# Performance work log

Hardware: AMD Instinct MI355X
Metric: run time of the kernel (lower is better)

The kernel has to match this reference:

```python
import jax, jax.numpy as jnp
import numpy as np

SPARSITY_PROB = 0.1
CAUSAL = True
B, H, S, D = 2, 16, 2048, 64


def _make_mask(key, seq_len, sparsity_prob, causal):
    # random_mask = rand < p, optionally AND causal tril, then force diagonal True
    m = jax.random.uniform(key, (seq_len, seq_len)) < sparsity_prob
    if causal:
        m = m & jnp.tril(jnp.ones((seq_len, seq_len), dtype=bool))
    idx = jnp.arange(seq_len)
    m = m.at[idx, idx].set(True)
    return m


def setup_inputs() -> dict:
    key = jax.random.key(0)
    kq, kk, kv, km = jax.random.split(key, 4)
    query = jax.random.normal(kq, (B, H, S, D), dtype=jnp.float32)
    k_ = jax.random.normal(kk, (B, H, S, D), dtype=jnp.float32)
    v_ = jax.random.normal(kv, (B, H, S, D), dtype=jnp.float32)
    mask = _make_mask(km, S, SPARSITY_PROB, CAUSAL)
    return {"query": query, "key": k_, "value": v_, "mask": mask}


def reference(query, key, value, mask):
    # Masked attention: softmax over the selected positions of each row is
    # mathematically identical to the per-row gather+softmax in the original.
    # mask: [S, S] bool, shared across batch and heads; every row has at least
    # the diagonal True, so no fully-masked rows.
    head_dim = query.shape[-1]
    scale = 1.0 / jnp.sqrt(jnp.asarray(head_dim, dtype=query.dtype))
    scores = jnp.einsum("bhqd,bhkd->bhqk", query, key) * scale  # [B,H,S,S]
    scores = jnp.where(mask[None, None, :, :], scores, -jnp.inf)
    attn = jax.nn.softmax(scores, axis=-1)
    return jnp.einsum("bhqk,bhkd->bhqd", attn, value)
```

## Files before the change

kernel.cpp:

```cpp
#include <hip/hip_runtime.h>
#include <hip/hip_bf16.h>

#define SEQ 2048
#define HD 64
#define NBH 32
#define SCALE 0.125f
#define QSC 0.18033688011112042f

typedef __attribute__((ext_vector_type(4)))  float    f32x4;
typedef __attribute__((ext_vector_type(16))) float    f32x16;
typedef __attribute__((ext_vector_type(8)))  short    bf16x8;
typedef __attribute__((ext_vector_type(4)))  unsigned u32x4;

__device__ inline short f2bf(float f) {
    unsigned u = __builtin_bit_cast(unsigned, f);
    unsigned r = u + 0x7FFFu + ((u >> 16) & 1u);
    return (short)(r >> 16);
}

__device__ inline unsigned cvt2(float lo, float hi) {
    unsigned d;
    asm("v_cvt_pk_bf16_f32 %0, %1, %2" : "=v"(d) : "v"(lo), "v"(hi));
    return d;
}

__global__ void detect_mask_kernel(const unsigned char* __restrict__ m, int n, int* flag) {
    if (threadIdx.x == 0) *flag = (m[n - 1] != 0) ? 1 : 4;
}

__global__ __launch_bounds__(256)
void prep_kernel(const unsigned char* __restrict__ m, const int* __restrict__ flag,
                 const float* __restrict__ K, const float* __restrict__ V,
                 unsigned* __restrict__ bits, short* __restrict__ Kb,
                 short* __restrict__ Vt) {
    __shared__ short t[64][65];
    const int b = blockIdx.x, tid = threadIdx.x;
    if (b < 512) {
        const int idx = b * 256 + tid;
        const int row = idx >> 6, w = idx & 63;
        const size_t base = (size_t)row * SEQ + w * 32;
        unsigned word = 0;
        if (*flag == 1) {
            #pragma unroll
            for (int i = 0; i < 32; ++i) word |= (unsigned)(m[base + i] != 0) << i;
        } else {
            const unsigned* m32 = (const unsigned*)m;
            #pragma unroll
            for (int i = 0; i < 32; ++i) word |= (unsigned)(m32[base + i] != 0) << i;
        }
        bits[(size_t)w * SEQ + row] = word;
    } else if (b < 2560) {
        const int g = (b - 512) * 256 + tid;
        const size_t i = (size_t)g * 8;
        f32x4 a = *(const f32x4*)(K + i);
        f32x4 c = *(const f32x4*)(K + i + 4);
        bf16x8 o;
        #pragma unroll
        for (int j = 0; j < 4; ++j) { o[j] = f2bf(a[j]); o[4 + j] = f2bf(c[j]); }
        const int row = g >> 3;
        const int c8  = g & 7;
        const int bh  = row >> 11;
        const int r   = row & 2047;
        const int tt  = r >> 5;
        const int la  = r & 31;
        *(bf16x8*)(Kb + ((size_t)bh * 64 + tt) * 2048 + (c8 * 32 + la) * 8) = o;
    } else {
        const int bb = b - 2560;
        const int s0 = (bb & 31) * 64, bh = bb >> 5;
        const float* Vb = V + (size_t)bh * SEQ * HD;
        const int sr = tid >> 6, d = tid & 63;
        #pragma unroll
        for (int i = 0; i < 16; ++i) {
            const int s = i * 4 + sr;
            t[s][d] = f2bf(Vb[(size_t)(s0 + s) * HD + d]);
        }
        __syncthreads();
        short* o = Vt + (size_t)bh * HD * SEQ;
        const int dr = tid >> 6, sl = tid & 63;
        #pragma unroll
        for (int i = 0; i < 16; ++i) {
            const int dd = i * 4 + dr;
            const int s = s0 + sl;
            const int k = s & 31;
            const int p = (k & ~12) | ((k & 8) >> 1) | ((k & 4) << 1);
            const int mm = ((dd >> 5) << 1) | (p >> 4);
            const int hh = (p >> 3) & 1;
            o[(size_t)(s >> 5) * 2048 + ((mm * 2 + hh) * 32 + (dd & 31)) * 8 + (p & 7)] = t[sl][dd];
        }
    }
}

__global__ __launch_bounds__(256, 2)
void attn_shared_kernel(const float* __restrict__ Q, const short* __restrict__ Kb,
                        const short* __restrict__ Vt, const unsigned* __restrict__ bitsT,
                        float* __restrict__ Out) {
    __shared__ __align__(16) short kbuf[2][2][2048];
    __shared__ __align__(16) short vbuf[2][2][2048];
    __shared__ short oacc[4][32][72];

    const int id   = blockIdx.x;
    const int bh   = id & 31;
    const int qg   = (id < 256) ? (15 - (id >> 5)) : ((id - 256) >> 5);
    const int tid  = threadIdx.x;
    const int wid  = tid >> 6;
    const int lane = tid & 63;
    const int la   = lane & 31;
    const int h    = lane >> 5;
    const int q0w  = qg * 128 + wid * 32;
    const int nt   = qg * 4 + 4;
    const size_t base = (size_t)bh * SEQ * HD;

    bf16x8 qf[4];
    {
        const float* qp = Q + base + (size_t)(q0w + la) * HD + h * 8;
        #pragma unroll
        for (int j = 0; j < 4; ++j) {
            f32x4 a0 = *(const f32x4*)(qp + j * 16);
            f32x4 a1 = *(const f32x4*)(qp + j * 16 + 4);
            #pragma unroll
            for (int i = 0; i < 4; ++i) {
                qf[j][i]     = f2bf(a0[i] * QSC);
                qf[j][4 + i] = f2bf(a1[i] * QSC);
            }
        }
    }

    f32x16 acc_o0 = {0,0,0,0,0,0,0,0,0,0,0,0,0,0,0,0};
    f32x16 acc_o1 = {0,0,0,0,0,0,0,0,0,0,0,0,0,0,0,0};
    float l_run = 0.f;

    const short* Ktg = Kb + (size_t)bh * 64 * 2048;
    const short* Vtg = Vt + (size_t)bh * 64 * 2048;
    const unsigned* bq = bitsT + q0w + la;
    const int bp = 4 * h;

    auto body = [&](const short* kb, const short* vb, unsigned mwx) {
        bf16x8 kfa = *(const bf16x8*)(kb + lane * 8);
        bf16x8 kfb = *(const bf16x8*)(kb + 512 + lane * 8);
        bf16x8 kfc = *(const bf16x8*)(kb + 1024 + lane * 8);
        bf16x8 kfd = *(const bf16x8*)(kb + 1536 + lane * 8);
        bf16x8 vf00 = *(const bf16x8*)(vb + lane * 8);
        bf16x8 vf01 = *(const bf16x8*)(vb + 512 + lane * 8);
        bf16x8 vf10 = *(const bf16x8*)(vb + 1024 + lane * 8);
        bf16x8 vf11 = *(const bf16x8*)(vb + 1536 + lane * 8);

        f32x16 sA = {0,0,0,0,0,0,0,0,0,0,0,0,0,0,0,0};
        f32x16 sB = {0,0,0,0,0,0,0,0,0,0,0,0,0,0,0,0};
        __builtin_amdgcn_s_setprio(1);
        sA = __builtin_amdgcn_mfma_f32_32x32x16_bf16(kfa, qf[0], sA, 0, 0, 0);
        sB = __builtin_amdgcn_mfma_f32_32x32x16_bf16(kfc, qf[2], sB, 0, 0, 0);
        sA = __builtin_amdgcn_mfma_f32_32x32x16_bf16(kfb, qf[1], sA, 0, 0, 0);
        sB = __builtin_amdgcn_mfma_f32_32x32x16_bf16(kfd, qf[3], sB, 0, 0, 0);
        __builtin_amdgcn_s_setprio(0);
        f32x16 s = sA + sB;

        #pragma unroll
        for (int r = 0; r < 16; ++r) {
            float e = __builtin_amdgcn_exp2f(s[r]);
            s[r] = ((mwx >> (bp + (r & 3) + 8 * (r >> 2))) & 1u) ? e : 0.f;
        }
        float ps = ((s[0] + s[1]) + (s[2] + s[3])) + ((s[4] + s[5]) + (s[6] + s[7]));
        ps += ((s[8] + s[9]) + (s[10] + s[11])) + ((s[12] + s[13]) + (s[14] + s[15]));
        l_run += ps;

        u32x4 t1 = {cvt2(s[0], s[1]),  cvt2(s[2], s[3]),
                    cvt2(s[4], s[5]),  cvt2(s[6], s[7])};
        u32x4 t2 = {cvt2(s[8], s[9]),  cvt2(s[10], s[11]),
                    cvt2(s[12], s[13]), cvt2(s[14], s[15])};
        bf16x8 pb1 = __builtin_bit_cast(bf16x8, t1);
        bf16x8 pb2 = __builtin_bit_cast(bf16x8, t2);

        __builtin_amdgcn_s_setprio(1);
        acc_o0 = __builtin_amdgcn_mfma_f32_32x32x16_bf16(vf00, pb1, acc_o0, 0, 0, 0);
        acc_o1 = __builtin_amdgcn_mfma_f32_32x32x16_bf16(vf10, pb1, acc_o1, 0, 0, 0);
        acc_o0 = __builtin_amdgcn_mfma_f32_32x32x16_bf16(vf01, pb2, acc_o0, 0, 0, 0);
        acc_o1 = __builtin_amdgcn_mfma_f32_32x32x16_bf16(vf11, pb2, acc_o1, 0, 0, 0);
        __builtin_amdgcn_s_setprio(0);
    };

    {
        bf16x8 k0 = *(const bf16x8*)(Ktg + (size_t)tid * 8);
        bf16x8 k1 = *(const bf16x8*)(Ktg + 2048 + (size_t)tid * 8);
        bf16x8 v0 = *(const bf16x8*)(Vtg + (size_t)tid * 8);
        bf16x8 v1 = *(const bf16x8*)(Vtg + 2048 + (size_t)tid * 8);
        *(bf16x8*)(&kbuf[0][0][0] + tid * 8) = k0;
        *(bf16x8*)(&kbuf[0][1][0] + tid * 8) = k1;
        *(bf16x8*)(&vbuf[0][0][0] + tid * 8) = v0;
        *(bf16x8*)(&vbuf[0][1][0] + tid * 8) = v1;
    }
    unsigned mw0 = bq[0];
    unsigned mw1 = bq[SEQ];

    int cur = 0;
    for (int t = 0; t < nt; t += 2) {
        __syncthreads();

        const int tn0 = (t + 2 < nt) ? t + 2 : t;
        const int tn1 = (t + 3 < nt) ? t + 3 : t;
        bf16x8 sk0 = *(const bf16x8*)(Ktg + (size_t)tn0 * 2048 + tid * 8);
        bf16x8 sk1 = *(const bf16x8*)(Ktg + (size_t)tn1 * 2048 + tid * 8);
        bf16x8 sv0 = *(const bf16x8*)(Vtg + (size_t)tn0 * 2048 + tid * 8);
        bf16x8 sv1 = *(const bf16x8*)(Vtg + (size_t)tn1 * 2048 + tid * 8);
        unsigned nmw0 = bq[(size_t)tn0 * SEQ];
        unsigned nmw1 = bq[(size_t)tn1 * SEQ];

        body(&kbuf[cur][0][0], &vbuf[cur][0][0], mw0);
        body(&kbuf[cur][1][0], &vbuf[cur][1][0], mw1);

        *(bf16x8*)(&kbuf[cur ^ 1][0][0] + tid * 8) = sk0;
        *(bf16x8*)(&kbuf[cur ^ 1][1][0] + tid * 8) = sk1;
        *(bf16x8*)(&vbuf[cur ^ 1][0][0] + tid * 8) = sv0;
        *(bf16x8*)(&vbuf[cur ^ 1][1][0] + tid * 8) = sv1;

        mw0 = nmw0; mw1 = nmw1;
        cur ^= 1;
    }

    {
        const float l_full = l_run + __shfl_xor(l_run, 32);
        const float invw = 1.f / l_full;
        unsigned short* orow = (unsigned short*)&oacc[wid][la][0];
        #pragma unroll
        for (int g = 0; g < 4; ++g) {
            const int d0 = 8 * g + 4 * h;
            unsigned w0 = cvt2(acc_o0[4 * g + 0] * invw, acc_o0[4 * g + 1] * invw);
            unsigned w1 = cvt2(acc_o0[4 * g + 2] * invw, acc_o0[4 * g + 3] * invw);
            unsigned w2 = cvt2(acc_o1[4 * g + 0] * invw, acc_o1[4 * g + 1] * invw);
            unsigned w3 = cvt2(acc_o1[4 * g + 2] * invw, acc_o1[4 * g + 3] * invw);
            *(unsigned*)&orow[d0]      = w0;
            *(unsigned*)&orow[d0 + 2]  = w1;
            *(unsigned*)&orow[d0 + 32] = w2;
            *(unsigned*)&orow[d0 + 34] = w3;
        }
    }
    __syncthreads();

    {
        const int q  = tid >> 3;
        const int dc = (tid & 7) * 8;
        #pragma unroll
        for (int k = 0; k < 4; ++k) {
            u32x4 pk = *(const u32x4*)&oacc[k][q][dc];
            float o[8];
            #pragma unroll
            for (int j = 0; j < 4; ++j) {
                o[2 * j]     = __builtin_bit_cast(float, (pk[j] & 0xFFFFu) << 16);
                o[2 * j + 1] = __builtin_bit_cast(float, pk[j] & 0xFFFF0000u);
            }
            float* op = Out + base + (size_t)(qg * 128 + k * 32 + q) * HD + dc;
            f32x4 o0v = {o[0], o[1], o[2], o[3]};
            f32x4 o1v = {o[4], o[5], o[6], o[7]};
            *(f32x4*)op       = o0v;
            *(f32x4*)(op + 4) = o1v;
        }
    }
}

__global__ __launch_bounds__(256)
void attn_kernel(const float* __restrict__ Q, const float* __restrict__ K,
                 const float* __restrict__ V, const unsigned char* __restrict__ mask,
                 const int* __restrict__ flag, float* __restrict__ Out) {
    __shared__ short plds[4][16][40];
    const int esz  = *flag;
    const int bh   = blockIdx.y;
    const int wid  = threadIdx.x >> 6;
    const int lane = threadIdx.x & 63;
    const int l16  = lane & 15;
    const int hi   = lane >> 4;
    const int q0   = blockIdx.x * 64 + wid * 16;
    const size_t base = (size_t)bh * SEQ * HD;
    const float* Qb = Q + base;
    const float* Kb = K + base;
    const float* Vb = V + base;
    const unsigned int* mask32 = (const unsigned int*)mask;
    bf16x8 qf[2];
    {
        const float* qp = Qb + (size_t)(q0 + l16) * HD + hi * 8;
        f32x4 a0 = *(const f32x4*)(qp);
        f32x4 a1 = *(const f32x4*)(qp + 4);
        f32x4 a2 = *(const f32x4*)(qp + 32);
        f32x4 a3 = *(const f32x4*)(qp + 36);
        #pragma unroll
        for (int i = 0; i < 4; ++i) {
            qf[0][i] = f2bf(a0[i]); qf[0][4 + i] = f2bf(a1[i]);
            qf[1][i] = f2bf(a2[i]); qf[1][4 + i] = f2bf(a3[i]);
        }
    }
    f32x4 acc_o[4] = {f32x4{0,0,0,0}, f32x4{0,0,0,0}, f32x4{0,0,0,0}, f32x4{0,0,0,0}};
    float m_run[4], l_run[4];
    #pragma unroll
    for (int j = 0; j < 4; ++j) { m_run[j] = -__builtin_inff(); l_run[j] = 0.f; }
    const int kv_end = q0 + 16;
    for (int kv = 0; kv < kv_end; kv += 32) {
        f32x4 acc_s[2] = {f32x4{0,0,0,0}, f32x4{0,0,0,0}};
        #pragma unroll
        for (int t = 0; t < 2; ++t) {
            const float* kp = Kb + (size_t)(kv + 16 * t + l16) * HD + hi * 8;
            f32x4 b0 = *(const f32x4*)(kp);
            f32x4 b1 = *(const f32x4*)(kp + 4);
            f32x4 b2 = *(const f32x4*)(kp + 32);
            f32x4 b3 = *(const f32x4*)(kp + 36);
            bf16x8 kf0, kf1;
            #pragma unroll
            for (int i = 0; i < 4; ++i) {
                kf0[i] = f2bf(b0[i]); kf0[4 + i] = f2bf(b1[i]);
                kf1[i] = f2bf(b2[i]); kf1[4 + i] = f2bf(b3[i]);
            }
            acc_s[t] = __builtin_amdgcn_mfma_f32_16x16x32_bf16(qf[0], kf0, acc_s[t], 0, 0, 0);
            acc_s[t] = __builtin_amdgcn_mfma_f32_16x16x32_bf16(qf[1], kf1, acc_s[t], 0, 0, 0);
        }
        float s[2][4];
        #pragma unroll
        for (int t = 0; t < 2; ++t) {
            const int k = kv + 16 * t + l16;
            #pragma unroll
            for (int j = 0; j < 4; ++j) {
                const int qrow = q0 + hi * 4 + j;
                const size_t midx = (size_t)qrow * SEQ + k;
                const bool mv = (esz == 1) ? (mask[midx] != 0) : (mask32[midx] != 0);
                s[t][j] = mv ? acc_s[t][j] * SCALE : -__builtin_inff();
            }
        }
        float mnew[4], r[4];
        #pragma unroll
        for (int j = 0; j < 4; ++j) {
            float v = fmaxf(s[0][j], s[1][j]);
            #pragma unroll
            for (int off = 1; off < 16; off <<= 1) v = fmaxf(v, __shfl_xor(v, off));
            mnew[j] = fmaxf(m_run[j], v);
            r[j] = (m_run[j] > -__builtin_inff()) ? __expf(m_run[j] - mnew[j]) : 0.f;
        }
        float p[2][4];
        #pragma unroll
        for (int j = 0; j < 4; ++j) {
            float ps = 0.f;
            #pragma unroll
            for (int t = 0; t < 2; ++t) {
                p[t][j] = (s[t][j] > -__builtin_inff()) ? __expf(s[t][j] - mnew[j]) : 0.f;
                ps += p[t][j];
            }
            #pragma unroll
            for (int off = 1; off < 16; off <<= 1) ps += __shfl_xor(ps, off);
            l_run[j] = l_run[j] * r[j] + ps;
            m_run[j] = mnew[j];
            #pragma unroll
            for (int t2 = 0; t2 < 4; ++t2) acc_o[t2][j] *= r[j];
        }
        #pragma unroll
        for (int t = 0; t < 2; ++t)
            #pragma unroll
            for (int j = 0; j < 4; ++j)
                plds[wid][hi * 4 + j][16 * t + l16] = f2bf(p[t][j]);
        bf16x8 pa = *(bf16x8*)&plds[wid][l16][hi * 8];
        #pragma unroll
        for (int t2 = 0; t2 < 4; ++t2) {
            const float* vp = Vb + (size_t)(kv + hi * 8) * HD + 16 * t2 + l16;
            bf16x8 vf;
            #pragma unroll
            for (int i = 0; i < 8; ++i) vf[i] = f2bf(vp[(size_t)i * HD]);
            acc_o[t2] = __builtin_amdgcn_mfma_f32_16x16x32_bf16(pa, vf, acc_o[t2], 0, 0, 0);
        }
    }
    #pragma unroll
    for (int j = 0; j < 4; ++j) {
        const float inv = 1.f / l_run[j];
        const int qrow = q0 + hi * 4 + j;
        float* op = Out + base + (size_t)qrow * HD + l16;
        #pragma unroll
        for (int t2 = 0; t2 < 4; ++t2) op[16 * t2] = acc_o[t2][j] * inv;
    }
}

extern "C" void kernel_launch(void* const* d_in, const int* in_sizes, int n_in,
                              void* d_out, int out_size, void* d_ws, size_t ws_size,
                              hipStream_t stream) {
    const float* Q = (const float*)d_in[0];
    const float* K = (const float*)d_in[1];
    const float* V = (const float*)d_in[2];
    const unsigned char* mask = (const unsigned char*)d_in[3];

    const size_t bitsB = (size_t)SEQ * (SEQ / 32) * 4;
    const size_t kvB   = (size_t)NBH * SEQ * HD * 2;
    const size_t need  = bitsB + 2 * kvB + 256;

    if (ws_size >= need) {
        unsigned* bits = (unsigned*)d_ws;
        short* Kb = (short*)((char*)d_ws + bitsB);
        short* Vt = (short*)((char*)d_ws + bitsB + kvB);
        int* flag = (int*)((char*)d_ws + bitsB + 2 * kvB);

        detect_mask_kernel<<<dim3(1), dim3(64), 0, stream>>>(mask, in_sizes[3], flag);
        prep_kernel<<<dim3(3584), dim3(256), 0, stream>>>(mask, flag, K, V, bits, Kb, Vt);
        attn_shared_kernel<<<dim3(512), dim3(256), 0, stream>>>(Q, Kb, Vt, bits, (float*)d_out);
    } else {
        int* flag = (int*)d_ws;
        detect_mask_kernel<<<dim3(1), dim3(64), 0, stream>>>(mask, in_sizes[3], flag);
        attn_kernel<<<dim3(SEQ / 64, NBH), dim3(256), 0, stream>>>(Q, K, V, mask, flag, (float*)d_out);
    }
}
```

Before: 58.43 us.

## Split attention KV range into halves with separate reduction kernel

Adds a split-KV attention path: each query group's causal key range is divided into two halves processed by separate blocks (1024 blocks, occupancy hint 4). Each block writes partial normalized outputs in bf16 and row sums to workspace, and a reduce kernel combines them weighted by the sums. The aim is more parallelism and better load balance across CUs for the causal workload. In exchange it adds an extra kernel launch, workspace traffic, and bf16 rounding of the partial outputs. The softmax skips the running max and relies on the prescaled exp2 scores staying bounded.

```diff
diff --git a/kernel.cpp b/kernel.cpp
--- a/kernel.cpp
+++ b/kernel.cpp
@@ -90,6 +90,213 @@
     }
 }
 
+__global__ __launch_bounds__(256, 4)
+void attn_half_kernel(const float* __restrict__ Q, const short* __restrict__ Kb,
+                      const short* __restrict__ Vt, const unsigned* __restrict__ bitsT,
+                      short* __restrict__ Oh_ws, float* __restrict__ l_ws) {
+    __shared__ __align__(16) short pool[16384];
+    short* kpool = pool;
+    short* vpool = pool + 8192;
+
+    const int id   = blockIdx.x;
+    const int bh   = id & 31;
+    const int s8   = (id >> 5) & 7;
+    const int g    = id >> 8;
+    int qg, half;
+    if (g == 0)      { qg = 15 - s8; half = 0; }
+    else if (g == 1) { qg = 8 + s8;  half = 1; }
+    else if (g == 2) { qg = 7 - s8;  half = 0; }
+    else             { qg = s8;      half = 1; }
+
+    const int tid  = threadIdx.x;
+    const int wid  = tid >> 6;
+    const int lane = tid & 63;
+    const int la   = lane & 31;
+    const int h    = lane >> 5;
+    const int q0w  = qg * 128 + wid * 32;
+    const int htiles = 2 * qg + 2;
+    const int tstart = half * htiles;
+    const int tend   = tstart + htiles;
+    const size_t base = (size_t)bh * SEQ * HD;
+
+    bf16x8 qf[4];
+    {
+        const float* qp = Q + base + (size_t)(q0w + la) * HD + h * 8;
+        #pragma unroll
+        for (int j = 0; j < 4; ++j) {
+            f32x4 a0 = *(const f32x4*)(qp + j * 16);
+            f32x4 a1 = *(const f32x4*)(qp + j * 16 + 4);
+            #pragma unroll
+            for (int i = 0; i < 4; ++i) {
+                qf[j][i]     = f2bf(a0[i] * QSC);
+                qf[j][4 + i] = f2bf(a1[i] * QSC);
+            }
+        }
+    }
+
+    f32x16 acc_o0 = {0,0,0,0,0,0,0,0,0,0,0,0,0,0,0,0};
+    f32x16 acc_o1 = {0,0,0,0,0,0,0,0,0,0,0,0,0,0,0,0};
+    float l_run = 0.f;
+
+    const short* Ktg = Kb + (size_t)bh * 64 * 2048;
+    const short* Vtg = Vt + (size_t)bh * 64 * 2048;
+    const unsigned* bq = bitsT + q0w + la;
+    const int bp = 4 * h;
+
+    auto body = [&](const short* kb, const short* vb, unsigned mwx) {
+        bf16x8 kfa = *(const bf16x8*)(kb + lane * 8);
+        bf16x8 kfb = *(const bf16x8*)(kb + 512 + lane * 8);
+        bf16x8 kfc = *(const bf16x8*)(kb + 1024 + lane * 8);
+        bf16x8 kfd = *(const bf16x8*)(kb + 1536 + lane * 8);
+        bf16x8 vf00 = *(const bf16x8*)(vb + lane * 8);
+        bf16x8 vf01 = *(const bf16x8*)(vb + 512 + lane * 8);
+        bf16x8 vf10 = *(const bf16x8*)(vb + 1024 + lane * 8);
+        bf16x8 vf11 = *(const bf16x8*)(vb + 1536 + lane * 8);
+
+        f32x16 sA = {0,0,0,0,0,0,0,0,0,0,0,0,0,0,0,0};
+        f32x16 sB = {0,0,0,0,0,0,0,0,0,0,0,0,0,0,0,0};
+        __builtin_amdgcn_s_setprio(1);
+        sA = __builtin_amdgcn_mfma_f32_32x32x16_bf16(kfa, qf[0], sA, 0, 0, 0);
+        sB = __builtin_amdgcn_mfma_f32_32x32x16_bf16(kfc, qf[2], sB, 0, 0, 0);
+        sA = __builtin_amdgcn_mfma_f32_32x32x16_bf16(kfb, qf[1], sA, 0, 0, 0);
+        sB = __builtin_amdgcn_mfma_f32_32x32x16_bf16(kfd, qf[3], sB, 0, 0, 0);
+        __builtin_amdgcn_s_setprio(0);
+        f32x16 s = sA + sB;
+
+        #pragma unroll
+        for (int r = 0; r < 16; ++r) {
+            float e = __builtin_amdgcn_exp2f(s[r]);
+            s[r] = ((mwx >> (bp + (r & 3) + 8 * (r >> 2))) & 1u) ? e : 0.f;
+        }
+        float ps = ((s[0] + s[1]) + (s[2] + s[3])) + ((s[4] + s[5]) + (s[6] + s[7]));
+        ps += ((s[8] + s[9]) + (s[10] + s[11])) + ((s[12] + s[13]) + (s[14] + s[15]));
+        l_run += ps;
+
+        u32x4 t1 = {cvt2(s[0], s[1]),  cvt2(s[2], s[3]),
+                    cvt2(s[4], s[5]),  cvt2(s[6], s[7])};
+        u32x4 t2 = {cvt2(s[8], s[9]),  cvt2(s[10], s[11]),
+                    cvt2(s[12], s[13]), cvt2(s[14], s[15])};
+        bf16x8 pb1 = __builtin_bit_cast(bf16x8, t1);
+        bf16x8 pb2 = __builtin_bit_cast(bf16x8, t2);
+
+        __builtin_amdgcn_s_setprio(1);
+        acc_o0 = __builtin_amdgcn_mfma_f32_32x32x16_bf16(vf00, pb1, acc_o0, 0, 0, 0);
+        acc_o1 = __builtin_amdgcn_mfma_f32_32x32x16_bf16(vf10, pb1, acc_o1, 0, 0, 0);
+        acc_o0 = __builtin_amdgcn_mfma_f32_32x32x16_bf16(vf01, pb2, acc_o0, 0, 0, 0);
+        acc_o1 = __builtin_amdgcn_mfma_f32_32x32x16_bf16(vf11, pb2, acc_o1, 0, 0, 0);
+        __builtin_amdgcn_s_setprio(0);
+    };
+
+    {
+        bf16x8 k0 = *(const bf16x8*)(Ktg + (size_t)tstart * 2048 + tid * 8);
+        bf16x8 k1 = *(const bf16x8*)(Ktg + (size_t)(tstart + 1) * 2048 + tid * 8);
+        bf16x8 v0 = *(const bf16x8*)(Vtg + (size_t)tstart * 2048 + tid * 8);
+        bf16x8 v1 = *(const bf16x8*)(Vtg + (size_t)(tstart + 1) * 2048 + tid * 8);
+        *(bf16x8*)(kpool + tid * 8) = k0;
+        *(bf16x8*)(kpool + 2048 + tid * 8) = k1;
+        *(bf16x8*)(vpool + tid * 8) = v0;
+        *(bf16x8*)(vpool + 2048 + tid * 8) = v1;
+    }
+    unsigned mw0 = bq[(size_t)tstart * SEQ];
+    unsigned mw1 = bq[(size_t)(tstart + 1) * SEQ];
+
+    int cur = 0;
+    for (int t = tstart; t < tend; t += 2) {
+        __syncthreads();
+
+        int tn0 = t + 2, tn1 = t + 3;
+        if (t + 2 >= tend) { tn0 = t; tn1 = t + 1; }
+        bf16x8 sk0 = *(const bf16x8*)(Ktg + (size_t)tn0 * 2048 + tid * 8);
+        bf16x8 sk1 = *(const bf16x8*)(Ktg + (size_t)tn1 * 2048 + tid * 8);
+        bf16x8 sv0 = *(const bf16x8*)(Vtg + (size_t)tn0 * 2048 + tid * 8);
+        bf16x8 sv1 = *(const bf16x8*)(Vtg + (size_t)tn1 * 2048 + tid * 8);
+        unsigned nmw0 = bq[(size_t)tn0 * SEQ];
+        unsigned nmw1 = bq[(size_t)tn1 * SEQ];
+
+        body(kpool + cur * 4096, vpool + cur * 4096, mw0);
+        body(kpool + cur * 4096 + 2048, vpool + cur * 4096 + 2048, mw1);
+
+        *(bf16x8*)(kpool + (cur ^ 1) * 4096 + tid * 8) = sk0;
+        *(bf16x8*)(kpool + (cur ^ 1) * 4096 + 2048 + tid * 8) = sk1;
+        *(bf16x8*)(vpool + (cur ^ 1) * 4096 + tid * 8) = sv0;
+        *(bf16x8*)(vpool + (cur ^ 1) * 4096 + 2048 + tid * 8) = sv1;
+
+        mw0 = nmw0; mw1 = nmw1;
+        cur ^= 1;
+    }
+
+    const int slot = (qg * 32 + bh) * 2 + half;
+
+    const float l_full = l_run + __shfl_xor(l_run, 32);
+    const float invw = (l_full > 0.f) ? (1.f / l_full) : 0.f;
+    if (h == 0) l_ws[(size_t)slot * 128 + wid * 32 + la] = l_full;
+
+    __syncthreads();
+
+    short (*oacc)[32][72] = (short (*)[32][72])pool;
+    {
+        unsigned short* orow = (unsigned short*)&oacc[wid][la][0];
+        #pragma unroll
+        for (int g2 = 0; g2 < 4; ++g2) {
+            const int d0 = 8 * g2 + 4 * h;
+            unsigned w0 = cvt2(acc_o0[4 * g2 + 0] * invw, acc_o0[4 * g2 + 1] * invw);
+            unsigned w1 = cvt2(acc_o0[4 * g2 + 2] * invw, acc_o0[4 * g2 + 3] * invw);
+            unsigned w2 = cvt2(acc_o1[4 * g2 + 0] * invw, acc_o1[4 * g2 + 1] * invw);
+            unsigned w3 = cvt2(acc_o1[4 * g2 + 2] * invw, acc_o1[4 * g2 + 3] * invw);
+            *(unsigned*)&orow[d0]      = w0;
+            *(unsigned*)&orow[d0 + 2]  = w1;
+            *(unsigned*)&orow[d0 + 32] = w2;
+            *(unsigned*)&orow[d0 + 34] = w3;
+        }
+    }
+    __syncthreads();
+
+    {
+        const int q  = tid >> 3;
+        const int dc = (tid & 7) * 8;
+        unsigned short* ob = (unsigned short*)Oh_ws + (size_t)slot * 8192;
+        #pragma unroll
+        for (int k = 0; k < 4; ++k) {
+            u32x4 pk = *(const u32x4*)&oacc[k][q][dc];
+            *(u32x4*)(ob + (k * 32 + q) * 64 + dc) = pk;
+        }
+    }
+}
+
+__global__ __launch_bounds__(256)
+void reduce_kernel(const short* __restrict__ Oh_ws, const float* __restrict__ l_ws,
+                   float* __restrict__ Out) {
+    const int id = blockIdx.x;
+    const int group = id >> 2;
+    const int sub = id & 3;
+    const int qg = group >> 5, bh = group & 31;
+    const int tid = threadIdx.x;
+    const int q  = sub * 32 + (tid >> 3);
+    const int dc = (tid & 7) * 8;
+    const size_t s0 = (size_t)(group * 2);
+
+    const float l0 = l_ws[s0 * 128 + q];
+    const float l1 = l_ws[(s0 + 1) * 128 + q];
+    const float inv = 1.f / (l0 + l1);
+    u32x4 p0 = *(const u32x4*)((const unsigned short*)Oh_ws + s0 * 8192 + q * 64 + dc);
+    u32x4 p1 = *(const u32x4*)((const unsigned short*)Oh_ws + (s0 + 1) * 8192 + q * 64 + dc);
+    float o[8];
+    #pragma unroll
+    for (int j = 0; j < 4; ++j) {
+        float a0 = __builtin_bit_cast(float, (p0[j] & 0xFFFFu) << 16);
+        float a1 = __builtin_bit_cast(float, p0[j] & 0xFFFF0000u);
+        float b0 = __builtin_bit_cast(float, (p1[j] & 0xFFFFu) << 16);
+        float b1 = __builtin_bit_cast(float, p1[j] & 0xFFFF0000u);
+        o[2 * j]     = (l0 * a0 + l1 * b0) * inv;
+        o[2 * j + 1] = (l0 * a1 + l1 * b1) * inv;
+    }
+    float* op = Out + (size_t)bh * SEQ * HD + (size_t)(qg * 128 + q) * HD + dc;
+    f32x4 o0v = {o[0], o[1], o[2], o[3]};
+    f32x4 o1v = {o[4], o[5], o[6], o[7]};
+    *(f32x4*)op       = o0v;
+    *(f32x4*)(op + 4) = o1v;
+}
+
 __global__ __launch_bounds__(256, 2)
 void attn_shared_kernel(const float* __restrict__ Q, const short* __restrict__ Kb,
                         const short* __restrict__ Vt, const unsigned* __restrict__ bitsT,
@@ -194,7 +401,6 @@
     int cur = 0;
     for (int t = 0; t < nt; t += 2) {
         __syncthreads();
-
         const int tn0 = (t + 2 < nt) ? t + 2 : t;
         const int tn1 = (t + 3 < nt) ? t + 3 : t;
         bf16x8 sk0 = *(const bf16x8*)(Ktg + (size_t)tn0 * 2048 + tid * 8);
@@ -381,9 +587,13 @@
 
     const size_t bitsB = (size_t)SEQ * (SEQ / 32) * 4;
     const size_t kvB   = (size_t)NBH * SEQ * HD * 2;
-    const size_t need  = bitsB + 2 * kvB + 256;
-
-    if (ws_size >= need) {
+    const size_t flagB = 256;
+    const size_t ohB   = (size_t)1024 * 8192 * 2;
+    const size_t lB    = (size_t)1024 * 128 * 4;
+    const size_t need_mono  = bitsB + 2 * kvB + flagB;
+    const size_t need_split = need_mono + ohB + lB;
+
+    if (ws_size >= need_mono) {
         unsigned* bits = (unsigned*)d_ws;
         short* Kb = (short*)((char*)d_ws + bitsB);
         short* Vt = (short*)((char*)d_ws + bitsB + kvB);
@@ -391,7 +601,15 @@
 
         detect_mask_kernel<<<dim3(1), dim3(64), 0, stream>>>(mask, in_sizes[3], flag);
         prep_kernel<<<dim3(3584), dim3(256), 0, stream>>>(mask, flag, K, V, bits, Kb, Vt);
-        attn_shared_kernel<<<dim3(512), dim3(256), 0, stream>>>(Q, Kb, Vt, bits, (float*)d_out);
+
+        if (ws_size >= need_split) {
+            short* Oh_ws = (short*)((char*)d_ws + need_mono);
+            float* l_ws  = (float*)((char*)d_ws + need_mono + ohB);
+            attn_half_kernel<<<dim3(1024), dim3(256), 0, stream>>>(Q, Kb, Vt, bits, Oh_ws, l_ws);
+            reduce_kernel<<<dim3(2048), dim3(256), 0, stream>>>(Oh_ws, l_ws, (float*)d_out);
+        } else {
+            attn_shared_kernel<<<dim3(512), dim3(256), 0, stream>>>(Q, Kb, Vt, bits, (float*)d_out);
+        }
     } else {
         int* flag = (int*)d_ws;
         detect_mask_kernel<<<dim3(1), dim3(64), 0, stream>>>(mask, in_sizes[3], flag);
```

Result: slower. 136.8 us (+134.2%).

## Drop mask-detect kernel launch, alias oacc onto K/V LDS pool, chain QK MFMAs

Applied to the files above, without the earlier changes.

Removes the separate single-thread detect_mask launch by having each mask-packing block read the last mask element itself to pick the byte or int32 path. The attention kernel now places the output staging buffer in the same shared-memory pool as the K/V double buffers, behind an added barrier, which cuts LDS use per block. The QK^T MFMAs are chained into a single accumulator instead of two summed ones. This saves a launch and LDS footprint at the cost of one more barrier and a serial MFMA dependency chain.

```diff
diff --git a/kernel.cpp b/kernel.cpp
--- a/kernel.cpp
+++ b/kernel.cpp
@@ -29,18 +29,19 @@
 }
 
 __global__ __launch_bounds__(256)
-void prep_kernel(const unsigned char* __restrict__ m, const int* __restrict__ flag,
+void prep_kernel(const unsigned char* __restrict__ m, int mn,
                  const float* __restrict__ K, const float* __restrict__ V,
                  unsigned* __restrict__ bits, short* __restrict__ Kb,
                  short* __restrict__ Vt) {
     __shared__ short t[64][65];
     const int b = blockIdx.x, tid = threadIdx.x;
     if (b < 512) {
+        const bool e1 = (m[mn - 1] != 0);
         const int idx = b * 256 + tid;
         const int row = idx >> 6, w = idx & 63;
         const size_t base = (size_t)row * SEQ + w * 32;
         unsigned word = 0;
-        if (*flag == 1) {
+        if (e1) {
             #pragma unroll
             for (int i = 0; i < 32; ++i) word |= (unsigned)(m[base + i] != 0) << i;
         } else {
@@ -91,12 +92,12 @@
 }
 
 __global__ __launch_bounds__(256, 2)
-void attn_shared_kernel(const float* __restrict__ Q, const short* __restrict__ Kb,
-                        const short* __restrict__ Vt, const unsigned* __restrict__ bitsT,
-                        float* __restrict__ Out) {
-    __shared__ __align__(16) short kbuf[2][2][2048];
-    __shared__ __align__(16) short vbuf[2][2][2048];
-    __shared__ short oacc[4][32][72];
+void attn_shared2_kernel(const float* __restrict__ Q, const short* __restrict__ Kb,
+                         const short* __restrict__ Vt, const unsigned* __restrict__ bitsT,
+                         float* __restrict__ Out) {
+    __shared__ __align__(16) short pool[16384];
+    short* kpool = pool;
+    short* vpool = pool + 8192;
 
     const int id   = blockIdx.x;
     const int bh   = id & 31;
@@ -144,15 +145,13 @@
         bf16x8 vf10 = *(const bf16x8*)(vb + 1024 + lane * 8);
         bf16x8 vf11 = *(const bf16x8*)(vb + 1536 + lane * 8);
 
-        f32x16 sA = {0,0,0,0,0,0,0,0,0,0,0,0,0,0,0,0};
-        f32x16 sB = {0,0,0,0,0,0,0,0,0,0,0,0,0,0,0,0};
+        f32x16 s = {0,0,0,0,0,0,0,0,0,0,0,0,0,0,0,0};
         __builtin_amdgcn_s_setprio(1);
-        sA = __builtin_amdgcn_mfma_f32_32x32x16_bf16(kfa, qf[0], sA, 0, 0, 0);
-        sB = __builtin_amdgcn_mfma_f32_32x32x16_bf16(kfc, qf[2], sB, 0, 0, 0);
-        sA = __builtin_amdgcn_mfma_f32_32x32x16_bf16(kfb, qf[1], sA, 0, 0, 0);
-        sB = __builtin_amdgcn_mfma_f32_32x32x16_bf16(kfd, qf[3], sB, 0, 0, 0);
+        s = __builtin_amdgcn_mfma_f32_32x32x16_bf16(kfa, qf[0], s, 0, 0, 0);
+        s = __builtin_amdgcn_mfma_f32_32x32x16_bf16(kfb, qf[1], s, 0, 0, 0);
+        s = __builtin_amdgcn_mfma_f32_32x32x16_bf16(kfc, qf[2], s, 0, 0, 0);
+        s = __builtin_amdgcn_mfma_f32_32x32x16_bf16(kfd, qf[3], s, 0, 0, 0);
         __builtin_amdgcn_s_setprio(0);
-        f32x16 s = sA + sB;
 
         #pragma unroll
         for (int r = 0; r < 16; ++r) {
@@ -183,10 +182,10 @@
         bf16x8 k1 = *(const bf16x8*)(Ktg + 2048 + (size_t)tid * 8);
         bf16x8 v0 = *(const bf16x8*)(Vtg + (size_t)tid * 8);
         bf16x8 v1 = *(const bf16x8*)(Vtg + 2048 + (size_t)tid * 8);
-        *(bf16x8*)(&kbuf[0][0][0] + tid * 8) = k0;
-        *(bf16x8*)(&kbuf[0][1][0] + tid * 8) = k1;
-        *(bf16x8*)(&vbuf[0][0][0] + tid * 8) = v0;
-        *(bf16x8*)(&vbuf[0][1][0] + tid * 8) = v1;
+        *(bf16x8*)(kpool + tid * 8) = k0;
+        *(bf16x8*)(kpool + 2048 + tid * 8) = k1;
+        *(bf16x8*)(vpool + tid * 8) = v0;
+        *(bf16x8*)(vpool + 2048 + tid * 8) = v1;
     }
     unsigned mw0 = bq[0];
     unsigned mw1 = bq[SEQ];
@@ -204,21 +203,25 @@
         unsigned nmw0 = bq[(size_t)tn0 * SEQ];
         unsigned nmw1 = bq[(size_t)tn1 * SEQ];
 
-        body(&kbuf[cur][0][0], &vbuf[cur][0][0], mw0);
-        body(&kbuf[cur][1][0], &vbuf[cur][1][0], mw1);
-
-        *(bf16x8*)(&kbuf[cur ^ 1][0][0] + tid * 8) = sk0;
-        *(bf16x8*)(&kbuf[cur ^ 1][1][0] + tid * 8) = sk1;
-        *(bf16x8*)(&vbuf[cur ^ 1][0][0] + tid * 8) = sv0;
-        *(bf16x8*)(&vbuf[cur ^ 1][1][0] + tid * 8) = sv1;
+        body(kpool + cur * 4096,        vpool + cur * 4096,        mw0);
+        body(kpool + cur * 4096 + 2048, vpool + cur * 4096 + 2048, mw1);
+
+        *(bf16x8*)(kpool + (cur ^ 1) * 4096 + tid * 8)        = sk0;
+        *(bf16x8*)(kpool + (cur ^ 1) * 4096 + 2048 + tid * 8) = sk1;
+        *(bf16x8*)(vpool + (cur ^ 1) * 4096 + tid * 8)        = sv0;
+        *(bf16x8*)(vpool + (cur ^ 1) * 4096 + 2048 + tid * 8) = sv1;
 
         mw0 = nmw0; mw1 = nmw1;
         cur ^= 1;
     }
 
+    const float l_full = l_run + __shfl_xor(l_run, 32);
+    const float invw = 1.f / l_full;
+
+    __syncthreads();
+
+    short (*oacc)[32][72] = (short (*)[32][72])pool;
     {
-        const float l_full = l_run + __shfl_xor(l_run, 32);
-        const float invw = 1.f / l_full;
         unsigned short* orow = (unsigned short*)&oacc[wid][la][0];
         #pragma unroll
         for (int g = 0; g < 4; ++g) {
@@ -387,11 +390,9 @@
         unsigned* bits = (unsigned*)d_ws;
         short* Kb = (short*)((char*)d_ws + bitsB);
         short* Vt = (short*)((char*)d_ws + bitsB + kvB);
-        int* flag = (int*)((char*)d_ws + bitsB + 2 * kvB);
-
-        detect_mask_kernel<<<dim3(1), dim3(64), 0, stream>>>(mask, in_sizes[3], flag);
-        prep_kernel<<<dim3(3584), dim3(256), 0, stream>>>(mask, flag, K, V, bits, Kb, Vt);
-        attn_shared_kernel<<<dim3(512), dim3(256), 0, stream>>>(Q, Kb, Vt, bits, (float*)d_out);
+
+        prep_kernel<<<dim3(3584), dim3(256), 0, stream>>>(mask, in_sizes[3], K, V, bits, Kb, Vt);
+        attn_shared2_kernel<<<dim3(512), dim3(256), 0, stream>>>(Q, Kb, Vt, bits, (float*)d_out);
     } else {
         int* flag = (int*)d_ws;
         detect_mask_kernel<<<dim3(1), dim3(64), 0, stream>>>(mask, in_sizes[3], flag);
```

Result: faster. 53.49 us (median of 3 runs) (-8.5%).
